# Kernel optimization log

Measured on AMD Instinct MI355X. Metric: run time of the kernel, lower is better.

Reference implementation:

```python
import jax, jax.numpy as jnp
import numpy as np

VOCAB, HID, EMB = 32000, 512, 100
DROPOUT = 0.3
BN_EPS = 1e-5


def setup_inputs() -> dict:
    key = jax.random.key(0)
    ks = jax.random.split(key, 12)
    B, T = 64, 512
    s = 1.0 / np.sqrt(HID)
    inp = {
        "x": jax.random.randint(ks[0], (B, T), 0, VOCAB),
        "emb_table": jax.random.normal(ks[1], (VOCAB, HID), jnp.float32) * 0.1,
        # PyTorch LSTMCell layout: weight_ih [4H, H], weight_hh [4H, H], gate order i,f,g,o
        "w_ih": jax.random.uniform(ks[2], (4 * HID, HID), jnp.float32, -s, s),
        "w_hh": jax.random.uniform(ks[3], (4 * HID, HID), jnp.float32, -s, s),
        "b_ih": jax.random.uniform(ks[4], (4 * HID,), jnp.float32, -s, s),
        "b_hh": jax.random.uniform(ks[5], (4 * HID,), jnp.float32, -s, s),
        "gamma": jnp.ones((HID,), jnp.float32),
        "beta": jnp.zeros((HID,), jnp.float32),
        "dec_w": jax.random.uniform(ks[6], (EMB, HID), jnp.float32, -s, s),
        "dec_b": jax.random.uniform(ks[7], (EMB,), jnp.float32, -s, s),
        # LockedDropout: one bernoulli(keep) mask shared across all timesteps
        "mask": jax.random.bernoulli(ks[8], 1.0 - DROPOUT, (B, HID)).astype(jnp.float32),
    }
    return inp


def reference(x, emb_table, w_ih, w_hh, b_ih, b_hh, gamma, beta, dec_w, dec_b, mask):
    embed = emb_table[x]                    # [B, T, H]
    xs = jnp.swapaxes(embed, 0, 1)          # [T, B, H]
    B = x.shape[0]
    keep = 1.0 - DROPOUT

    def step(carry, x_t):
        h, c = carry
        gates = x_t @ w_ih.T + b_ih + h @ w_hh.T + b_hh     # [B, 4H]
        i, f, g, o = jnp.split(gates, 4, axis=-1)
        i = jax.nn.sigmoid(i)
        f = jax.nn.sigmoid(f)
        g = jnp.tanh(g)
        o = jax.nn.sigmoid(o)
        c = f * c + i * g
        h = o * jnp.tanh(c)
        # BatchNorm1d in training mode: per-step batch stats (biased variance)
        mu = jnp.mean(h, axis=0)
        var = jnp.mean((h - mu) ** 2, axis=0)
        hn = (h - mu) * jax.lax.rsqrt(var + BN_EPS) * gamma + beta
        hd = hn * mask / keep                # LockedDropout, fixed mask
        out = hd @ dec_w.T + dec_b           # [B, EMB]
        return (h, c), out

    h0 = jnp.zeros((B, HID), embed.dtype)
    c0 = jnp.zeros((B, HID), embed.dtype)
    _, outs = jax.lax.scan(step, (h0, c0), xs)   # [T, B, EMB]
    # MaxPool1d with kernel == T over time axis -> max over T
    return jnp.max(outs, axis=0)                  # [B, EMB]
```

## Files before the change

### kernel.cpp

```cpp
#include <hip/hip_runtime.h>
#include <hip/hip_bf16.h>

#define TSEQ  512
#define BATCH 64
#define HIDN  512
#define EMBD  100
#define NWG   64

typedef __attribute__((ext_vector_type(8))) short short8;
typedef __attribute__((ext_vector_type(4))) float f32x4;
typedef unsigned int u32;

#define A_OFF   0ull
#define HD_OFF  33554432ull
#define HB_OFF  67108864ull
#define FLG_OFF 67239936ull
#define KEY_OFF 67244032ull
#define DW_OFF  67269632ull
#define ZERO_SPAN 160768ull

static __device__ __forceinline__ unsigned short f2bfbits(float f) {
    u32 u = __float_as_uint(f);
    u32 r = (u + 0x7fffu + ((u >> 16) & 1u)) >> 16;
    return (unsigned short)r;
}

static __device__ __forceinline__ float sigf(float x) {
    return __builtin_amdgcn_rcpf(1.0f + __expf(-x));
}
static __device__ __forceinline__ float tanhfast(float x) {
    float t = __expf(-2.0f * fabsf(x));
    float r = (1.0f - t) * __builtin_amdgcn_rcpf(1.0f + t);
    return copysignf(r, x);
}

__global__ void k_dw(const float* __restrict__ dw, unsigned short* __restrict__ dwb) {
    int i = blockIdx.x * 256 + threadIdx.x;
    float v = (i < EMBD * HIDN) ? dw[i] : 0.0f;
    dwb[i] = f2bfbits(v);
}

__global__ void k_embed(const int* __restrict__ x, const float* __restrict__ emb,
                        unsigned short* __restrict__ A) {
    int g = blockIdx.x * 256 + threadIdx.x;
    int k8 = g & 63;
    int bt = g >> 6;
    int b  = bt & 63;
    int t  = bt >> 6;
    int row = x[b * TSEQ + t];
    const float4* src = reinterpret_cast<const float4*>(emb + (size_t)row * HIDN + k8 * 8);
    float4 v0 = src[0], v1 = src[1];
    short8 s;
    s[0] = (short)f2bfbits(v0.x); s[1] = (short)f2bfbits(v0.y);
    s[2] = (short)f2bfbits(v0.z); s[3] = (short)f2bfbits(v0.w);
    s[4] = (short)f2bfbits(v1.x); s[5] = (short)f2bfbits(v1.y);
    s[6] = (short)f2bfbits(v1.z); s[7] = (short)f2bfbits(v1.w);
    *reinterpret_cast<short8*>(A + (size_t)g * 8) = s;
}

__launch_bounds__(512)
__global__ void k_lstm(const float* __restrict__ wih, const float* __restrict__ whh,
                       const float* __restrict__ bih, const float* __restrict__ bhh,
                       const float* __restrict__ gamma, const float* __restrict__ beta,
                       const float* __restrict__ mask,
                       const unsigned short* __restrict__ A,
                       unsigned short* __restrict__ hbuf,
                       unsigned short* __restrict__ hd,
                       u32* __restrict__ flg) {
    const int tid  = threadIdx.x;
    const int wg   = blockIdx.x;
    const int lane = tid & 63;
    const int w    = tid >> 6;
    const int mb   = w & 3;
    const int kh   = w >> 2;

    __shared__ float gbuf[2][64][33];
    __shared__ __align__(16) unsigned short hstage[64][8];
    __shared__ __align__(16) unsigned short hdstage[2][64][8];

    const int l15 = lane & 15;
    const int lk8 = (lane >> 4) * 8;

    const float* wsrc = kh ? whh : wih;
    short8 bfr[16][2];
    #pragma unroll
    for (int kk = 0; kk < 16; ++kk) {
        #pragma unroll
        for (int nb = 0; nb < 2; ++nb) {
            int nl   = nb * 16 + l15;
            int gate = nl >> 3, jl = nl & 7;
            int ng   = gate * HIDN + wg * 8 + jl;
            int kl   = kk * 32 + lk8;
            const float* p = wsrc + (size_t)ng * HIDN + kl;
            short8 bb;
            #pragma unroll
            for (int e = 0; e < 8; ++e) bb[e] = (short)f2bfbits(p[e]);
            bfr[kk][nb] = bb;
        }
    }

    const int jj = wg * 8 + w;
    const float bias_i = bih[jj]          + bhh[jj];
    const float bias_f = bih[512 + jj]    + bhh[512 + jj];
    const float bias_g = bih[1024 + jj]   + bhh[1024 + jj];
    const float bias_o = bih[1536 + jj]   + bhh[1536 + jj];
    const float gam = gamma[jj], bet = beta[jj];
    const float mk  = mask[(size_t)lane * HIDN + jj] * (1.0f / 0.7f);
    float c = 0.0f;

    const int arow = mb * 16 + l15;
    const u32* fp = flg + lane * 16;

    {
        float* g1 = &gbuf[1][0][0];
        for (int i = tid; i < 64 * 33; i += 512) g1[i] = 0.0f;
    }
    __syncthreads();
    if (kh == 0) {
        const unsigned short* abase = A + (size_t)arow * HIDN;
        f32x4 acc0 = {0.f,0.f,0.f,0.f}, acc1 = {0.f,0.f,0.f,0.f};
        #pragma unroll
        for (int kk = 0; kk < 16; ++kk) {
            short8 a = *reinterpret_cast<const short8*>(abase + kk * 32 + lk8);
            acc0 = __builtin_amdgcn_mfma_f32_16x16x32_bf16(a, bfr[kk][0], acc0, 0, 0, 0);
            acc1 = __builtin_amdgcn_mfma_f32_16x16x32_bf16(a, bfr[kk][1], acc1, 0, 0, 0);
        }
        #pragma unroll
        for (int r = 0; r < 4; ++r) {
            int row = mb * 16 + (lane >> 4) * 4 + r;
            gbuf[0][row][l15]      = acc0[r];
            gbuf[0][row][16 + l15] = acc1[r];
        }
    }
    __syncthreads();

    for (int s = 0; s < TSEQ; ++s) {
        float gi = gbuf[0][lane][w]      + gbuf[1][lane][w]      + bias_i;
        float gf = gbuf[0][lane][8 + w]  + gbuf[1][lane][8 + w]  + bias_f;
        float gg = gbuf[0][lane][16 + w] + gbuf[1][lane][16 + w] + bias_g;
        float go = gbuf[0][lane][24 + w] + gbuf[1][lane][24 + w] + bias_o;
        float iv = sigf(gi), fv = sigf(gf), gv = tanhfast(gg), ov = sigf(go);
        c = fv * c + iv * gv;
        float h = ov * tanhfast(c);
        hstage[lane][w] = f2bfbits(h);
        __syncthreads();

        const int sb = (s + 1) & 1;

        if (s != TSEQ - 1 && w == 0) {
            short8 hv = *reinterpret_cast<const short8*>(&hstage[lane][0]);
            unsigned short* dst = hbuf + (size_t)sb * 32768 + (size_t)wg * 512 + lane * 8;
            asm volatile("global_store_dwordx4 %0, %1, off sc1" :: "v"(dst), "v"(hv) : "memory");
        }

        {
            float s1 = h, s2 = h * h;
            #pragma unroll
            for (int m = 1; m < 64; m <<= 1) {
                s1 += __shfl_xor(s1, m, 64);
                s2 += __shfl_xor(s2, m, 64);
            }
            float mu  = s1 * (1.0f / 64.0f);
            float var = s2 * (1.0f / 64.0f) - mu * mu;
            float hn  = (h - mu) * rsqrtf(var + 1e-5f) * gam + bet;
            hdstage[s & 1][lane][w] = f2bfbits(hn * mk);
        }

        if (s != TSEQ - 1 && w == 0) {
            asm volatile("s_waitcnt vmcnt(0)" ::: "memory");
            if (lane == 0) {
                u32 fv = (u32)(s + 1);
                const u32* myf = flg + wg * 16;
                asm volatile("global_store_dword %0, %1, off sc1" :: "v"(myf), "v"(fv) : "memory");
            }
        }

        if (s != TSEQ - 1) {
            if (kh == 0) {
                const unsigned short* abase = A + ((size_t)(s + 1) * 64 + arow) * HIDN;
                f32x4 acc0 = {0.f,0.f,0.f,0.f}, acc1 = {0.f,0.f,0.f,0.f};
                #pragma unroll
                for (int kk = 0; kk < 16; ++kk) {
                    short8 a = *reinterpret_cast<const short8*>(abase + kk * 32 + lk8);
                    acc0 = __builtin_amdgcn_mfma_f32_16x16x32_bf16(a, bfr[kk][0], acc0, 0, 0, 0);
                    acc1 = __builtin_amdgcn_mfma_f32_16x16x32_bf16(a, bfr[kk][1], acc1, 0, 0, 0);
                }
                #pragma unroll
                for (int r = 0; r < 4; ++r) {
                    int row = mb * 16 + (lane >> 4) * 4 + r;
                    gbuf[0][row][l15]      = acc0[r];
                    gbuf[0][row][16 + l15] = acc1[r];
                }
            } else {
                const u32 tgt = (u32)(s + 1);
                u32 v;
                do {
                    asm volatile("global_load_dword %0, %1, off sc1"
                                 : "=v"(v) : "v"(fp) : "memory");
                    asm volatile("s_waitcnt vmcnt(0)" ::: "memory");
                } while (!__all((int)(v >= tgt)));
                __builtin_amdgcn_sched_barrier(0);
                short8 hf[16];
                #pragma unroll
                for (int kk = 0; kk < 16; ++kk) {
                    const unsigned short* p = hbuf + (size_t)sb * 32768
                        + (size_t)(kk * 4 + (lane >> 4)) * 512 + arow * 8;
                    asm volatile("global_load_dwordx4 %0, %1, off sc1"
                                 : "=v"(hf[kk]) : "v"(p) : "memory");
                }
                asm volatile("s_waitcnt vmcnt(0)" ::: "memory");
                __builtin_amdgcn_sched_barrier(0);
                f32x4 acc0 = {0.f,0.f,0.f,0.f}, acc1 = {0.f,0.f,0.f,0.f};
                #pragma unroll
                for (int kk = 0; kk < 16; ++kk) {
                    acc0 = __builtin_amdgcn_mfma_f32_16x16x32_bf16(hf[kk], bfr[kk][0], acc0, 0, 0, 0);
                    acc1 = __builtin_amdgcn_mfma_f32_16x16x32_bf16(hf[kk], bfr[kk][1], acc1, 0, 0, 0);
                }
                #pragma unroll
                for (int r = 0; r < 4; ++r) {
                    int row = mb * 16 + (lane >> 4) * 4 + r;
                    gbuf[1][row][l15]      = acc0[r];
                    gbuf[1][row][16 + l15] = acc1[r];
                }
            }
        }
        __syncthreads();

        if (w == 1) {
            short8 dv = *reinterpret_cast<const short8*>(&hdstage[s & 1][lane][0]);
            *reinterpret_cast<short8*>(hd + ((size_t)s * 64 + lane) * HIDN + wg * 8) = dv;
        }
    }
}

__launch_bounds__(256)
__global__ void k_decode(const unsigned short* __restrict__ hd,
                         const unsigned short* __restrict__ dwb,
                         u32* __restrict__ key) {
    const int t    = blockIdx.x;
    const int tid  = threadIdx.x;
    const int lane = tid & 63;
    const int w    = tid >> 6;
    const int l15  = lane & 15;
    const int lk8  = (lane >> 4) * 8;
    const int brow = w * 16 + l15;

    const unsigned short* abase = hd + ((size_t)t * 64 + brow) * HIDN;
    f32x4 acc[7];
    #pragma unroll
    for (int nb = 0; nb < 7; ++nb) acc[nb] = (f32x4){0.f, 0.f, 0.f, 0.f};

    #pragma unroll
    for (int kk = 0; kk < 16; ++kk) {
        short8 a = *reinterpret_cast<const short8*>(abase + kk * 32 + lk8);
        #pragma unroll
        for (int nb = 0; nb < 7; ++nb) {
            short8 b = *reinterpret_cast<const short8*>(
                dwb + (size_t)(nb * 16 + l15) * HIDN + kk * 32 + lk8);
            acc[nb] = __builtin_amdgcn_mfma_f32_16x16x32_bf16(a, b, acc[nb], 0, 0, 0);
        }
    }
    #pragma unroll
    for (int nb = 0; nb < 7; ++nb) {
        int n = nb * 16 + l15;
        if (n < EMBD) {
            #pragma unroll
            for (int r = 0; r < 4; ++r) {
                int b = w * 16 + (lane >> 4) * 4 + r;
                u32 u  = __float_as_uint(acc[nb][r]);
                u32 kv = (u & 0x80000000u) ? ~u : (u | 0x80000000u);
                atomicMax(&key[b * EMBD + n], kv);
            }
        }
    }
}

__global__ void k_final(const u32* __restrict__ key, const float* __restrict__ db,
                        float* __restrict__ out) {
    int i = blockIdx.x * 256 + threadIdx.x;
    if (i < BATCH * EMBD) {
        u32 k = key[i];
        u32 u = (k & 0x80000000u) ? (k & 0x7fffffffu) : ~k;
        out[i] = __uint_as_float(u) + db[i % EMBD];
    }
}

extern "C" void kernel_launch(void* const* d_in, const int* in_sizes, int n_in,
                              void* d_out, int out_size, void* d_ws, size_t ws_size,
                              hipStream_t stream) {
    const int*   x   = (const int*)d_in[0];
    const float* emb = (const float*)d_in[1];
    const float* wih = (const float*)d_in[2];
    const float* whh = (const float*)d_in[3];
    const float* bih = (const float*)d_in[4];
    const float* bhh = (const float*)d_in[5];
    const float* gam = (const float*)d_in[6];
    const float* bet = (const float*)d_in[7];
    const float* dw  = (const float*)d_in[8];
    const float* db  = (const float*)d_in[9];
    const float* msk = (const float*)d_in[10];

    char* ws = (char*)d_ws;
    unsigned short* A   = (unsigned short*)(ws + A_OFF);
    unsigned short* hd  = (unsigned short*)(ws + HD_OFF);
    unsigned short* hb  = (unsigned short*)(ws + HB_OFF);
    u32*            flg = (u32*)(ws + FLG_OFF);
    u32*            key = (u32*)(ws + KEY_OFF);
    unsigned short* dwb = (unsigned short*)(ws + DW_OFF);

    hipMemsetAsync(ws + HB_OFF, 0, ZERO_SPAN, stream);
    k_dw    <<<224,  256, 0, stream>>>(dw, dwb);
    k_embed <<<8192, 256, 0, stream>>>(x, emb, A);
    k_lstm  <<<NWG,  512, 0, stream>>>(wih, whh, bih, bhh, gam, bet, msk, A, hb, hd, flg);
    k_decode<<<TSEQ, 256, 0, stream>>>(hd, dwb, key);
    k_final <<<25,   256, 0, stream>>>(key, db, (float*)d_out);
}
```

Before: 2.118 ms.

## Embed step tags in h exchange and split K across all waves

Each hidden-state word is now stored interleaved with the step number, so consumers can check tags on the data itself. That replaces a separate flag poll followed by a dependent load, and the per-workgroup flag remains only as a fallback after several retries. The work is also re-partitioned so all 8 waves each handle a quarter of K for both the input and recurrent GEMMs, instead of half the waves doing input and half doing recurrent. The next step's input loads and the h loads are issued early, before the batch-norm reduction. The exchange buffer doubles in size and the gate sum now reads four partial buffers, and the tag check relies on 16-byte stores being observed atomically.

```diff
diff --git a/kernel.cpp b/kernel.cpp
--- a/kernel.cpp
+++ b/kernel.cpp
@@ -10,14 +10,15 @@
 typedef __attribute__((ext_vector_type(8))) short short8;
 typedef __attribute__((ext_vector_type(4))) float f32x4;
 typedef unsigned int u32;
+typedef __attribute__((ext_vector_type(4))) u32 u32x4;
 
 #define A_OFF   0ull
 #define HD_OFF  33554432ull
 #define HB_OFF  67108864ull
-#define FLG_OFF 67239936ull
-#define KEY_OFF 67244032ull
-#define DW_OFF  67269632ull
-#define ZERO_SPAN 160768ull
+#define FLG_OFF 67371008ull
+#define KEY_OFF 67375104ull
+#define DW_OFF  67400704ull
+#define ZERO_SPAN 291840ull
 
 static __device__ __forceinline__ unsigned short f2bfbits(float f) {
     u32 u = __float_as_uint(f);
@@ -58,44 +59,45 @@
     *reinterpret_cast<short8*>(A + (size_t)g * 8) = s;
 }
 
-__launch_bounds__(512)
+__launch_bounds__(512, 1)
 __global__ void k_lstm(const float* __restrict__ wih, const float* __restrict__ whh,
                        const float* __restrict__ bih, const float* __restrict__ bhh,
                        const float* __restrict__ gamma, const float* __restrict__ beta,
                        const float* __restrict__ mask,
                        const unsigned short* __restrict__ A,
-                       unsigned short* __restrict__ hbuf,
+                       u32* __restrict__ hx,
                        unsigned short* __restrict__ hd,
                        u32* __restrict__ flg) {
     const int tid  = threadIdx.x;
     const int wg   = blockIdx.x;
     const int lane = tid & 63;
     const int w    = tid >> 6;
-    const int mb   = w & 3;
-    const int kh   = w >> 2;
-
-    __shared__ float gbuf[2][64][33];
+    const int mh   = w & 1;
+    const int kq   = w >> 1;
+
+    __shared__ float gbuf[4][64][33];
     __shared__ __align__(16) unsigned short hstage[64][8];
     __shared__ __align__(16) unsigned short hdstage[2][64][8];
 
     const int l15 = lane & 15;
     const int lk8 = (lane >> 4) * 8;
 
-    const float* wsrc = kh ? whh : wih;
-    short8 bfr[16][2];
-    #pragma unroll
-    for (int kk = 0; kk < 16; ++kk) {
+    short8 bfrA[4][2], bfrH[4][2];
+    #pragma unroll
+    for (int kk = 0; kk < 4; ++kk) {
         #pragma unroll
         for (int nb = 0; nb < 2; ++nb) {
             int nl   = nb * 16 + l15;
             int gate = nl >> 3, jl = nl & 7;
             int ng   = gate * HIDN + wg * 8 + jl;
-            int kl   = kk * 32 + lk8;
-            const float* p = wsrc + (size_t)ng * HIDN + kl;
-            short8 bb;
-            #pragma unroll
-            for (int e = 0; e < 8; ++e) bb[e] = (short)f2bfbits(p[e]);
-            bfr[kk][nb] = bb;
+            int kl   = kq * 128 + kk * 32 + lk8;
+            const float* pa = wih + (size_t)ng * HIDN + kl;
+            const float* ph = whh + (size_t)ng * HIDN + kl;
+            short8 ba, bh;
+            #pragma unroll
+            for (int e = 0; e < 8; ++e) { ba[e] = (short)f2bfbits(pa[e]); bh[e] = (short)f2bfbits(ph[e]); }
+            bfrA[kk][nb] = ba;
+            bfrH[kk][nb] = bh;
         }
     }
 
@@ -108,49 +110,80 @@
     const float mk  = mask[(size_t)lane * HIDN + jj] * (1.0f / 0.7f);
     float c = 0.0f;
 
-    const int arow = mb * 16 + l15;
-    const u32* fp = flg + lane * 16;
-
-    {
-        float* g1 = &gbuf[1][0][0];
-        for (int i = tid; i < 64 * 33; i += 512) g1[i] = 0.0f;
-    }
-    __syncthreads();
-    if (kh == 0) {
-        const unsigned short* abase = A + (size_t)arow * HIDN;
-        f32x4 acc0 = {0.f,0.f,0.f,0.f}, acc1 = {0.f,0.f,0.f,0.f};
+    const int arow0 = mh * 32 + l15;
+    const u32* fpoll = flg + lane * 16;
+
+    #pragma unroll
+    for (int f = 0; f < 2; ++f) {
+        const unsigned short* abase = A + (size_t)(arow0 + f * 16) * HIDN + kq * 128;
+        f32x4 a0 = {0.f,0.f,0.f,0.f}, a1 = {0.f,0.f,0.f,0.f};
         #pragma unroll
-        for (int kk = 0; kk < 16; ++kk) {
+        for (int kk = 0; kk < 4; ++kk) {
             short8 a = *reinterpret_cast<const short8*>(abase + kk * 32 + lk8);
-            acc0 = __builtin_amdgcn_mfma_f32_16x16x32_bf16(a, bfr[kk][0], acc0, 0, 0, 0);
-            acc1 = __builtin_amdgcn_mfma_f32_16x16x32_bf16(a, bfr[kk][1], acc1, 0, 0, 0);
+            a0 = __builtin_amdgcn_mfma_f32_16x16x32_bf16(a, bfrA[kk][0], a0, 0, 0, 0);
+            a1 = __builtin_amdgcn_mfma_f32_16x16x32_bf16(a, bfrA[kk][1], a1, 0, 0, 0);
         }
         #pragma unroll
         for (int r = 0; r < 4; ++r) {
-            int row = mb * 16 + (lane >> 4) * 4 + r;
-            gbuf[0][row][l15]      = acc0[r];
-            gbuf[0][row][16 + l15] = acc1[r];
+            int row = mh * 32 + f * 16 + (lane >> 4) * 4 + r;
+            gbuf[kq][row][l15]      = a0[r];
+            gbuf[kq][row][16 + l15] = a1[r];
         }
     }
     __syncthreads();
 
     for (int s = 0; s < TSEQ; ++s) {
-        float gi = gbuf[0][lane][w]      + gbuf[1][lane][w]      + bias_i;
-        float gf = gbuf[0][lane][8 + w]  + gbuf[1][lane][8 + w]  + bias_f;
-        float gg = gbuf[0][lane][16 + w] + gbuf[1][lane][16 + w] + bias_g;
-        float go = gbuf[0][lane][24 + w] + gbuf[1][lane][24 + w] + bias_o;
+        float gi = gbuf[0][lane][w]      + gbuf[1][lane][w]
+                 + gbuf[2][lane][w]      + gbuf[3][lane][w]      + bias_i;
+        float gf = gbuf[0][lane][8 + w]  + gbuf[1][lane][8 + w]
+                 + gbuf[2][lane][8 + w]  + gbuf[3][lane][8 + w]  + bias_f;
+        float gg = gbuf[0][lane][16 + w] + gbuf[1][lane][16 + w]
+                 + gbuf[2][lane][16 + w] + gbuf[3][lane][16 + w] + bias_g;
+        float go = gbuf[0][lane][24 + w] + gbuf[1][lane][24 + w]
+                 + gbuf[2][lane][24 + w] + gbuf[3][lane][24 + w] + bias_o;
         float iv = sigf(gi), fv = sigf(gf), gv = tanhfast(gg), ov = sigf(go);
         c = fv * c + iv * gv;
         float h = ov * tanhfast(c);
         hstage[lane][w] = f2bfbits(h);
         __syncthreads();
 
-        const int sb = (s + 1) & 1;
-
-        if (s != TSEQ - 1 && w == 0) {
-            short8 hv = *reinterpret_cast<const short8*>(&hstage[lane][0]);
-            unsigned short* dst = hbuf + (size_t)sb * 32768 + (size_t)wg * 512 + lane * 8;
-            asm volatile("global_store_dwordx4 %0, %1, off sc1" :: "v"(dst), "v"(hv) : "memory");
+        const int last = (s == TSEQ - 1);
+        const int sb   = (s + 1) & 1;
+        const u32 tgt  = (u32)(s + 1);
+
+        short8 af[4][2];
+        u32x4  g0[4][2], g1[4][2];
+
+        if (!last) {
+            if (w == 0) {
+                const u32* hrow = reinterpret_cast<const u32*>(&hstage[lane][0]);
+                u32 a0 = hrow[0], a1 = hrow[1], a2 = hrow[2], a3 = hrow[3];
+                u32x4 q0 = {a0, tgt, a1, tgt};
+                u32x4 q1 = {a2, tgt, a3, tgt};
+                u32* dst = hx + (((size_t)sb * NWG + wg) * 64 + lane) * 8;
+                asm volatile("global_store_dwordx4 %0, %1, off sc1" :: "v"(dst), "v"(q0) : "memory");
+                asm volatile("global_store_dwordx4 %0, %1, off sc1" :: "v"(dst + 4), "v"(q1) : "memory");
+            }
+            #pragma unroll
+            for (int f = 0; f < 2; ++f) {
+                const unsigned short* abase =
+                    A + ((size_t)(s + 1) * 64 + arow0 + f * 16) * HIDN + kq * 128;
+                #pragma unroll
+                for (int kk = 0; kk < 4; ++kk) {
+                    const unsigned short* p = abase + kk * 32 + lk8;
+                    asm volatile("global_load_dwordx4 %0, %1, off" : "=v"(af[kk][f]) : "v"(p) : "memory");
+                }
+            }
+            #pragma unroll
+            for (int f = 0; f < 2; ++f) {
+                #pragma unroll
+                for (int kk = 0; kk < 4; ++kk) {
+                    int wgp = kq * 16 + kk * 4 + (lane >> 4);
+                    const u32* p = hx + (((size_t)sb * NWG + wgp) * 64 + arow0 + f * 16) * 8;
+                    asm volatile("global_load_dwordx4 %0, %1, off sc1" : "=v"(g0[kk][f]) : "v"(p) : "memory");
+                    asm volatile("global_load_dwordx4 %0, %1, off sc1" : "=v"(g1[kk][f]) : "v"(p + 4) : "memory");
+                }
+            }
         }
 
         {
@@ -166,61 +199,101 @@
             hdstage[s & 1][lane][w] = f2bfbits(hn * mk);
         }
 
-        if (s != TSEQ - 1 && w == 0) {
+        if (!last) {
             asm volatile("s_waitcnt vmcnt(0)" ::: "memory");
-            if (lane == 0) {
-                u32 fv = (u32)(s + 1);
+            __builtin_amdgcn_sched_barrier(0);
+            if (w == 0 && lane == 0) {
                 const u32* myf = flg + wg * 16;
-                asm volatile("global_store_dword %0, %1, off sc1" :: "v"(myf), "v"(fv) : "memory");
-            }
-        }
-
-        if (s != TSEQ - 1) {
-            if (kh == 0) {
-                const unsigned short* abase = A + ((size_t)(s + 1) * 64 + arow) * HIDN;
-                f32x4 acc0 = {0.f,0.f,0.f,0.f}, acc1 = {0.f,0.f,0.f,0.f};
-                #pragma unroll
-                for (int kk = 0; kk < 16; ++kk) {
-                    short8 a = *reinterpret_cast<const short8*>(abase + kk * 32 + lk8);
-                    acc0 = __builtin_amdgcn_mfma_f32_16x16x32_bf16(a, bfr[kk][0], acc0, 0, 0, 0);
-                    acc1 = __builtin_amdgcn_mfma_f32_16x16x32_bf16(a, bfr[kk][1], acc1, 0, 0, 0);
-                }
-                #pragma unroll
-                for (int r = 0; r < 4; ++r) {
-                    int row = mb * 16 + (lane >> 4) * 4 + r;
-                    gbuf[0][row][l15]      = acc0[r];
-                    gbuf[0][row][16 + l15] = acc1[r];
-                }
-            } else {
-                const u32 tgt = (u32)(s + 1);
+                asm volatile("global_store_dword %0, %1, off sc1" :: "v"(myf), "v"(tgt) : "memory");
+            }
+
+            int ok;
+            {
+                int o = 1;
+                #pragma unroll
+                for (int f = 0; f < 2; ++f)
+                    #pragma unroll
+                    for (int kk = 0; kk < 4; ++kk)
+                        o &= (g0[kk][f].y == tgt) & (g0[kk][f].w == tgt)
+                           & (g1[kk][f].y == tgt) & (g1[kk][f].w == tgt);
+                ok = __all(o);
+            }
+            #pragma unroll 1
+            for (int att = 0; att < 6 && !ok; ++att) {
+                #pragma unroll
+                for (int f = 0; f < 2; ++f) {
+                    #pragma unroll
+                    for (int kk = 0; kk < 4; ++kk) {
+                        int wgp = kq * 16 + kk * 4 + (lane >> 4);
+                        const u32* p = hx + (((size_t)sb * NWG + wgp) * 64 + arow0 + f * 16) * 8;
+                        if ((g0[kk][f].y != tgt) | (g0[kk][f].w != tgt))
+                            asm volatile("global_load_dwordx4 %0, %1, off sc1" : "=v"(g0[kk][f]) : "v"(p) : "memory");
+                        if ((g1[kk][f].y != tgt) | (g1[kk][f].w != tgt))
+                            asm volatile("global_load_dwordx4 %0, %1, off sc1" : "=v"(g1[kk][f]) : "v"(p + 4) : "memory");
+                    }
+                }
+                asm volatile("s_waitcnt vmcnt(0)" ::: "memory");
+                __builtin_amdgcn_sched_barrier(0);
+                int o = 1;
+                #pragma unroll
+                for (int f = 0; f < 2; ++f)
+                    #pragma unroll
+                    for (int kk = 0; kk < 4; ++kk)
+                        o &= (g0[kk][f].y == tgt) & (g0[kk][f].w == tgt)
+                           & (g1[kk][f].y == tgt) & (g1[kk][f].w == tgt);
+                ok = __all(o);
+            }
+            if (!ok) {
                 u32 v;
                 do {
-                    asm volatile("global_load_dword %0, %1, off sc1"
-                                 : "=v"(v) : "v"(fp) : "memory");
+                    asm volatile("global_load_dword %0, %1, off sc1" : "=v"(v) : "v"(fpoll) : "memory");
                     asm volatile("s_waitcnt vmcnt(0)" ::: "memory");
                 } while (!__all((int)(v >= tgt)));
                 __builtin_amdgcn_sched_barrier(0);
-                short8 hf[16];
-                #pragma unroll
-                for (int kk = 0; kk < 16; ++kk) {
-                    const unsigned short* p = hbuf + (size_t)sb * 32768
-                        + (size_t)(kk * 4 + (lane >> 4)) * 512 + arow * 8;
-                    asm volatile("global_load_dwordx4 %0, %1, off sc1"
-                                 : "=v"(hf[kk]) : "v"(p) : "memory");
+                #pragma unroll
+                for (int f = 0; f < 2; ++f) {
+                    #pragma unroll
+                    for (int kk = 0; kk < 4; ++kk) {
+                        int wgp = kq * 16 + kk * 4 + (lane >> 4);
+                        const u32* p = hx + (((size_t)sb * NWG + wgp) * 64 + arow0 + f * 16) * 8;
+                        asm volatile("global_load_dwordx4 %0, %1, off sc1" : "=v"(g0[kk][f]) : "v"(p) : "memory");
+                        asm volatile("global_load_dwordx4 %0, %1, off sc1" : "=v"(g1[kk][f]) : "v"(p + 4) : "memory");
+                    }
                 }
                 asm volatile("s_waitcnt vmcnt(0)" ::: "memory");
                 __builtin_amdgcn_sched_barrier(0);
-                f32x4 acc0 = {0.f,0.f,0.f,0.f}, acc1 = {0.f,0.f,0.f,0.f};
-                #pragma unroll
-                for (int kk = 0; kk < 16; ++kk) {
-                    acc0 = __builtin_amdgcn_mfma_f32_16x16x32_bf16(hf[kk], bfr[kk][0], acc0, 0, 0, 0);
-                    acc1 = __builtin_amdgcn_mfma_f32_16x16x32_bf16(hf[kk], bfr[kk][1], acc1, 0, 0, 0);
-                }
+            }
+
+            f32x4 acc[2][2];
+            #pragma unroll
+            for (int f = 0; f < 2; ++f)
+                #pragma unroll
+                for (int nb = 0; nb < 2; ++nb) acc[f][nb] = (f32x4){0.f,0.f,0.f,0.f};
+            #pragma unroll
+            for (int f = 0; f < 2; ++f) {
+                #pragma unroll
+                for (int kk = 0; kk < 4; ++kk) {
+                    acc[f][0] = __builtin_amdgcn_mfma_f32_16x16x32_bf16(af[kk][f], bfrA[kk][0], acc[f][0], 0, 0, 0);
+                    acc[f][1] = __builtin_amdgcn_mfma_f32_16x16x32_bf16(af[kk][f], bfrA[kk][1], acc[f][1], 0, 0, 0);
+                }
+            }
+            #pragma unroll
+            for (int f = 0; f < 2; ++f) {
+                #pragma unroll
+                for (int kk = 0; kk < 4; ++kk) {
+                    u32x4 q = {g0[kk][f].x, g0[kk][f].z, g1[kk][f].x, g1[kk][f].z};
+                    short8 a = *reinterpret_cast<short8*>(&q);
+                    acc[f][0] = __builtin_amdgcn_mfma_f32_16x16x32_bf16(a, bfrH[kk][0], acc[f][0], 0, 0, 0);
+                    acc[f][1] = __builtin_amdgcn_mfma_f32_16x16x32_bf16(a, bfrH[kk][1], acc[f][1], 0, 0, 0);
+                }
+            }
+            #pragma unroll
+            for (int f = 0; f < 2; ++f) {
                 #pragma unroll
                 for (int r = 0; r < 4; ++r) {
-                    int row = mb * 16 + (lane >> 4) * 4 + r;
-                    gbuf[1][row][l15]      = acc0[r];
-                    gbuf[1][row][16 + l15] = acc1[r];
+                    int row = mh * 32 + f * 16 + (lane >> 4) * 4 + r;
+                    gbuf[kq][row][l15]      = acc[f][0][r];
+                    gbuf[kq][row][16 + l15] = acc[f][1][r];
                 }
             }
         }
@@ -303,7 +376,7 @@
     char* ws = (char*)d_ws;
     unsigned short* A   = (unsigned short*)(ws + A_OFF);
     unsigned short* hd  = (unsigned short*)(ws + HD_OFF);
-    unsigned short* hb  = (unsigned short*)(ws + HB_OFF);
+    u32*            hx  = (u32*)(ws + HB_OFF);
     u32*            flg = (u32*)(ws + FLG_OFF);
     u32*            key = (u32*)(ws + KEY_OFF);
     unsigned short* dwb = (unsigned short*)(ws + DW_OFF);
@@ -311,7 +384,7 @@
     hipMemsetAsync(ws + HB_OFF, 0, ZERO_SPAN, stream);
     k_dw    <<<224,  256, 0, stream>>>(dw, dwb);
     k_embed <<<8192, 256, 0, stream>>>(x, emb, A);
-    k_lstm  <<<NWG,  512, 0, stream>>>(wih, whh, bih, bhh, gam, bet, msk, A, hb, hd, flg);
+    k_lstm  <<<NWG,  512, 0, stream>>>(wih, whh, bih, bhh, gam, bet, msk, A, hx, hd, flg);
     k_decode<<<TSEQ, 256, 0, stream>>>(hd, dwb, key);
     k_final <<<25,   256, 0, stream>>>(key, db, (float*)d_out);
 }
```

After: 2.585 ms. 1.22x slower.

## Split LSTM workgroups by batch and hidden slices; move BatchNorm into decode kernel

Applied to the files above, without the earlier changes.

The recurrent kernel now gives each workgroup 16 batch rows and 32 hidden units across all four gates, instead of 8 hidden units for all 64 batch rows. Each workgroup then only waits on the 16 peers that share its batch slice rather than all 64. The per-step BatchNorm and dropout, which needed a cross-batch reduction, move out of the serial loop. A new k_bnd kernel computes per-timestep batch statistics from bf16 hidden states in shared memory before the decoder GEMM. The trade-off is that BN statistics now come from bf16-rounded h, and the decode kernel does extra shared-memory and normalisation work.

```diff
diff --git a/kernel.cpp b/kernel.cpp
--- a/kernel.cpp
+++ b/kernel.cpp
@@ -24,7 +24,9 @@
     u32 r = (u + 0x7fffu + ((u >> 16) & 1u)) >> 16;
     return (unsigned short)r;
 }
-
+static __device__ __forceinline__ float bf2f(unsigned short b) {
+    return __uint_as_float(((u32)b) << 16);
+}
 static __device__ __forceinline__ float sigf(float x) {
     return __builtin_amdgcn_rcpf(1.0f + __expf(-x));
 }
@@ -61,22 +63,21 @@
 __launch_bounds__(512)
 __global__ void k_lstm(const float* __restrict__ wih, const float* __restrict__ whh,
                        const float* __restrict__ bih, const float* __restrict__ bhh,
-                       const float* __restrict__ gamma, const float* __restrict__ beta,
-                       const float* __restrict__ mask,
                        const unsigned short* __restrict__ A,
                        unsigned short* __restrict__ hbuf,
                        unsigned short* __restrict__ hd,
                        u32* __restrict__ flg) {
     const int tid  = threadIdx.x;
     const int wg   = blockIdx.x;
+    const int g    = wg & 3;
+    const int m    = wg >> 2;
     const int lane = tid & 63;
     const int w    = tid >> 6;
-    const int mb   = w & 3;
+    const int nbw  = w & 3;
     const int kh   = w >> 2;
 
-    __shared__ float gbuf[2][64][33];
-    __shared__ __align__(16) unsigned short hstage[64][8];
-    __shared__ __align__(16) unsigned short hdstage[2][64][8];
+    __shared__ float gbuf[2][16][132];
+    __shared__ __align__(16) unsigned short hstage[2][16][32];
 
     const int l15 = lane & 15;
     const int lk8 = (lane >> 4) * 8;
@@ -87,11 +88,8 @@
     for (int kk = 0; kk < 16; ++kk) {
         #pragma unroll
         for (int nb = 0; nb < 2; ++nb) {
-            int nl   = nb * 16 + l15;
-            int gate = nl >> 3, jl = nl & 7;
-            int ng   = gate * HIDN + wg * 8 + jl;
-            int kl   = kk * 32 + lk8;
-            const float* p = wsrc + (size_t)ng * HIDN + kl;
+            int jrow = nbw * HIDN + m * 32 + nb * 16 + l15;
+            const float* p = wsrc + (size_t)jrow * HIDN + kk * 32 + lk8;
             short8 bb;
             #pragma unroll
             for (int e = 0; e < 8; ++e) bb[e] = (short)f2bfbits(p[e]);
@@ -99,160 +97,178 @@
         }
     }
 
-    const int jj = wg * 8 + w;
-    const float bias_i = bih[jj]          + bhh[jj];
-    const float bias_f = bih[512 + jj]    + bhh[512 + jj];
-    const float bias_g = bih[1024 + jj]   + bhh[1024 + jj];
-    const float bias_o = bih[1536 + jj]   + bhh[1536 + jj];
-    const float gam = gamma[jj], bet = beta[jj];
-    const float mk  = mask[(size_t)lane * HIDN + jj] * (1.0f / 0.7f);
+    const int prow = tid >> 5;
+    const int pcol = tid & 31;
+    const int jj   = m * 32 + pcol;
+    const float bias_i = bih[jj]           + bhh[jj];
+    const float bias_f = bih[512 + jj]     + bhh[512 + jj];
+    const float bias_g = bih[1024 + jj]    + bhh[1024 + jj];
+    const float bias_o = bih[1536 + jj]    + bhh[1536 + jj];
     float c = 0.0f;
 
-    const int arow = mb * 16 + l15;
-    const u32* fp = flg + lane * 16;
+    const int arow = g * 16 + l15;
+    const u32* fpoll = flg + ((size_t)g * 16 + (lane & 15)) * 16;
 
     {
         float* g1 = &gbuf[1][0][0];
-        for (int i = tid; i < 64 * 33; i += 512) g1[i] = 0.0f;
+        for (int i = tid; i < 16 * 132; i += 512) g1[i] = 0.0f;
     }
     __syncthreads();
     if (kh == 0) {
         const unsigned short* abase = A + (size_t)arow * HIDN;
-        f32x4 acc0 = {0.f,0.f,0.f,0.f}, acc1 = {0.f,0.f,0.f,0.f};
+        f32x4 a0 = {0.f,0.f,0.f,0.f}, a1 = {0.f,0.f,0.f,0.f};
         #pragma unroll
         for (int kk = 0; kk < 16; ++kk) {
             short8 a = *reinterpret_cast<const short8*>(abase + kk * 32 + lk8);
-            acc0 = __builtin_amdgcn_mfma_f32_16x16x32_bf16(a, bfr[kk][0], acc0, 0, 0, 0);
-            acc1 = __builtin_amdgcn_mfma_f32_16x16x32_bf16(a, bfr[kk][1], acc1, 0, 0, 0);
+            a0 = __builtin_amdgcn_mfma_f32_16x16x32_bf16(a, bfr[kk][0], a0, 0, 0, 0);
+            a1 = __builtin_amdgcn_mfma_f32_16x16x32_bf16(a, bfr[kk][1], a1, 0, 0, 0);
         }
         #pragma unroll
         for (int r = 0; r < 4; ++r) {
-            int row = mb * 16 + (lane >> 4) * 4 + r;
-            gbuf[0][row][l15]      = acc0[r];
-            gbuf[0][row][16 + l15] = acc1[r];
+            int crow = (lane >> 4) * 4 + r;
+            gbuf[0][crow][nbw * 32 + l15]      = a0[r];
+            gbuf[0][crow][nbw * 32 + 16 + l15] = a1[r];
         }
     }
     __syncthreads();
 
     for (int s = 0; s < TSEQ; ++s) {
-        float gi = gbuf[0][lane][w]      + gbuf[1][lane][w]      + bias_i;
-        float gf = gbuf[0][lane][8 + w]  + gbuf[1][lane][8 + w]  + bias_f;
-        float gg = gbuf[0][lane][16 + w] + gbuf[1][lane][16 + w] + bias_g;
-        float go = gbuf[0][lane][24 + w] + gbuf[1][lane][24 + w] + bias_o;
+        float gi = gbuf[0][prow][pcol]      + gbuf[1][prow][pcol]      + bias_i;
+        float gf = gbuf[0][prow][32 + pcol] + gbuf[1][prow][32 + pcol] + bias_f;
+        float gg = gbuf[0][prow][64 + pcol] + gbuf[1][prow][64 + pcol] + bias_g;
+        float go = gbuf[0][prow][96 + pcol] + gbuf[1][prow][96 + pcol] + bias_o;
         float iv = sigf(gi), fv = sigf(gf), gv = tanhfast(gg), ov = sigf(go);
         c = fv * c + iv * gv;
         float h = ov * tanhfast(c);
-        hstage[lane][w] = f2bfbits(h);
+        hstage[s & 1][prow][pcol] = f2bfbits(h);
         __syncthreads();
 
-        const int sb = (s + 1) & 1;
-
-        if (s != TSEQ - 1 && w == 0) {
-            short8 hv = *reinterpret_cast<const short8*>(&hstage[lane][0]);
-            unsigned short* dst = hbuf + (size_t)sb * 32768 + (size_t)wg * 512 + lane * 8;
+        const int last = (s == TSEQ - 1);
+        const int sb   = (s + 1) & 1;
+        const u32 tgt  = (u32)(s + 1);
+
+        if (!last && w == 0) {
+            int r0 = lane >> 2, pc = (lane & 3) * 8;
+            short8 hv = *reinterpret_cast<const short8*>(&hstage[s & 1][r0][pc]);
+            unsigned short* dst = hbuf + ((size_t)(sb * 4 + g) * 16 + r0) * HIDN + m * 32 + pc;
             asm volatile("global_store_dwordx4 %0, %1, off sc1" :: "v"(dst), "v"(hv) : "memory");
-        }
-
-        {
-            float s1 = h, s2 = h * h;
-            #pragma unroll
-            for (int m = 1; m < 64; m <<= 1) {
-                s1 += __shfl_xor(s1, m, 64);
-                s2 += __shfl_xor(s2, m, 64);
-            }
-            float mu  = s1 * (1.0f / 64.0f);
-            float var = s2 * (1.0f / 64.0f) - mu * mu;
-            float hn  = (h - mu) * rsqrtf(var + 1e-5f) * gam + bet;
-            hdstage[s & 1][lane][w] = f2bfbits(hn * mk);
-        }
-
-        if (s != TSEQ - 1 && w == 0) {
             asm volatile("s_waitcnt vmcnt(0)" ::: "memory");
             if (lane == 0) {
-                u32 fv = (u32)(s + 1);
-                const u32* myf = flg + wg * 16;
-                asm volatile("global_store_dword %0, %1, off sc1" :: "v"(myf), "v"(fv) : "memory");
+                const u32* myf = flg + ((size_t)g * 16 + m) * 16;
+                asm volatile("global_store_dword %0, %1, off sc1" :: "v"(myf), "v"(tgt) : "memory");
             }
         }
 
-        if (s != TSEQ - 1) {
+        if (w == 1) {
+            int r0 = lane >> 2, pc = (lane & 3) * 8;
+            short8 dv = *reinterpret_cast<const short8*>(&hstage[s & 1][r0][pc]);
+            *reinterpret_cast<short8*>(
+                hd + ((size_t)s * 64 + g * 16 + r0) * HIDN + m * 32 + pc) = dv;
+        }
+
+        if (!last) {
             if (kh == 0) {
                 const unsigned short* abase = A + ((size_t)(s + 1) * 64 + arow) * HIDN;
-                f32x4 acc0 = {0.f,0.f,0.f,0.f}, acc1 = {0.f,0.f,0.f,0.f};
+                f32x4 a0 = {0.f,0.f,0.f,0.f}, a1 = {0.f,0.f,0.f,0.f};
                 #pragma unroll
                 for (int kk = 0; kk < 16; ++kk) {
                     short8 a = *reinterpret_cast<const short8*>(abase + kk * 32 + lk8);
-                    acc0 = __builtin_amdgcn_mfma_f32_16x16x32_bf16(a, bfr[kk][0], acc0, 0, 0, 0);
-                    acc1 = __builtin_amdgcn_mfma_f32_16x16x32_bf16(a, bfr[kk][1], acc1, 0, 0, 0);
+                    a0 = __builtin_amdgcn_mfma_f32_16x16x32_bf16(a, bfr[kk][0], a0, 0, 0, 0);
+                    a1 = __builtin_amdgcn_mfma_f32_16x16x32_bf16(a, bfr[kk][1], a1, 0, 0, 0);
                 }
                 #pragma unroll
                 for (int r = 0; r < 4; ++r) {
-                    int row = mb * 16 + (lane >> 4) * 4 + r;
-                    gbuf[0][row][l15]      = acc0[r];
-                    gbuf[0][row][16 + l15] = acc1[r];
+                    int crow = (lane >> 4) * 4 + r;
+                    gbuf[0][crow][nbw * 32 + l15]      = a0[r];
+                    gbuf[0][crow][nbw * 32 + 16 + l15] = a1[r];
                 }
             } else {
-                const u32 tgt = (u32)(s + 1);
                 u32 v;
                 do {
                     asm volatile("global_load_dword %0, %1, off sc1"
-                                 : "=v"(v) : "v"(fp) : "memory");
+                                 : "=v"(v) : "v"(fpoll) : "memory");
                     asm volatile("s_waitcnt vmcnt(0)" ::: "memory");
                 } while (!__all((int)(v >= tgt)));
                 __builtin_amdgcn_sched_barrier(0);
+                const unsigned short* hbase = hbuf + ((size_t)(sb * 4 + g) * 16 + l15) * HIDN;
                 short8 hf[16];
                 #pragma unroll
                 for (int kk = 0; kk < 16; ++kk) {
-                    const unsigned short* p = hbuf + (size_t)sb * 32768
-                        + (size_t)(kk * 4 + (lane >> 4)) * 512 + arow * 8;
+                    const unsigned short* p = hbase + kk * 32 + lk8;
                     asm volatile("global_load_dwordx4 %0, %1, off sc1"
                                  : "=v"(hf[kk]) : "v"(p) : "memory");
                 }
                 asm volatile("s_waitcnt vmcnt(0)" ::: "memory");
                 __builtin_amdgcn_sched_barrier(0);
-                f32x4 acc0 = {0.f,0.f,0.f,0.f}, acc1 = {0.f,0.f,0.f,0.f};
+                f32x4 a0 = {0.f,0.f,0.f,0.f}, a1 = {0.f,0.f,0.f,0.f};
                 #pragma unroll
                 for (int kk = 0; kk < 16; ++kk) {
-                    acc0 = __builtin_amdgcn_mfma_f32_16x16x32_bf16(hf[kk], bfr[kk][0], acc0, 0, 0, 0);
-                    acc1 = __builtin_amdgcn_mfma_f32_16x16x32_bf16(hf[kk], bfr[kk][1], acc1, 0, 0, 0);
+                    a0 = __builtin_amdgcn_mfma_f32_16x16x32_bf16(hf[kk], bfr[kk][0], a0, 0, 0, 0);
+                    a1 = __builtin_amdgcn_mfma_f32_16x16x32_bf16(hf[kk], bfr[kk][1], a1, 0, 0, 0);
                 }
                 #pragma unroll
                 for (int r = 0; r < 4; ++r) {
-                    int row = mb * 16 + (lane >> 4) * 4 + r;
-                    gbuf[1][row][l15]      = acc0[r];
-                    gbuf[1][row][16 + l15] = acc1[r];
+                    int crow = (lane >> 4) * 4 + r;
+                    gbuf[1][crow][nbw * 32 + l15]      = a0[r];
+                    gbuf[1][crow][nbw * 32 + 16 + l15] = a1[r];
                 }
             }
         }
         __syncthreads();
-
-        if (w == 1) {
-            short8 dv = *reinterpret_cast<const short8*>(&hdstage[s & 1][lane][0]);
-            *reinterpret_cast<short8*>(hd + ((size_t)s * 64 + lane) * HIDN + wg * 8) = dv;
-        }
     }
 }
 
 __launch_bounds__(256)
-__global__ void k_decode(const unsigned short* __restrict__ hd,
-                         const unsigned short* __restrict__ dwb,
-                         u32* __restrict__ key) {
-    const int t    = blockIdx.x;
-    const int tid  = threadIdx.x;
+__global__ void k_bnd(const unsigned short* __restrict__ hd,
+                      const unsigned short* __restrict__ dwb,
+                      const float* __restrict__ gamma, const float* __restrict__ beta,
+                      const float* __restrict__ mask,
+                      u32* __restrict__ key) {
+    const int t   = blockIdx.x;
+    const int tid = threadIdx.x;
+    __shared__ __align__(16) unsigned short hs[64][520];
+
+    for (int ch = tid; ch < 4096; ch += 256) {
+        int row = ch >> 6, c8 = (ch & 63) * 8;
+        short8 v = *reinterpret_cast<const short8*>(hd + ((size_t)t * 64 + row) * HIDN + c8);
+        *reinterpret_cast<short8*>(&hs[row][c8]) = v;
+    }
+    __syncthreads();
+
+    {
+        int c0 = tid * 2;
+        float s10 = 0.f, s20 = 0.f, s11 = 0.f, s21 = 0.f;
+        for (int r = 0; r < 64; ++r) {
+            float x0 = bf2f(hs[r][c0]), x1 = bf2f(hs[r][c0 + 1]);
+            s10 += x0; s20 += x0 * x0;
+            s11 += x1; s21 += x1 * x1;
+        }
+        float mu0 = s10 * (1.0f / 64.0f), var0 = s20 * (1.0f / 64.0f) - mu0 * mu0;
+        float mu1 = s11 * (1.0f / 64.0f), var1 = s21 * (1.0f / 64.0f) - mu1 * mu1;
+        float sc0 = gamma[c0]     * rsqrtf(var0 + 1e-5f);
+        float sc1 = gamma[c0 + 1] * rsqrtf(var1 + 1e-5f);
+        float sh0 = beta[c0]     - mu0 * sc0;
+        float sh1 = beta[c0 + 1] - mu1 * sc1;
+        for (int r = 0; r < 64; ++r) {
+            float2 mk = *reinterpret_cast<const float2*>(&mask[(size_t)r * HIDN + c0]);
+            float y0 = (bf2f(hs[r][c0])     * sc0 + sh0) * mk.x * (1.0f / 0.7f);
+            float y1 = (bf2f(hs[r][c0 + 1]) * sc1 + sh1) * mk.y * (1.0f / 0.7f);
+            hs[r][c0]     = f2bfbits(y0);
+            hs[r][c0 + 1] = f2bfbits(y1);
+        }
+    }
+    __syncthreads();
+
     const int lane = tid & 63;
     const int w    = tid >> 6;
     const int l15  = lane & 15;
     const int lk8  = (lane >> 4) * 8;
-    const int brow = w * 16 + l15;
-
-    const unsigned short* abase = hd + ((size_t)t * 64 + brow) * HIDN;
     f32x4 acc[7];
     #pragma unroll
     for (int nb = 0; nb < 7; ++nb) acc[nb] = (f32x4){0.f, 0.f, 0.f, 0.f};
-
     #pragma unroll
     for (int kk = 0; kk < 16; ++kk) {
-        short8 a = *reinterpret_cast<const short8*>(abase + kk * 32 + lk8);
+        short8 a = *reinterpret_cast<const short8*>(&hs[w * 16 + l15][kk * 32 + lk8]);
         #pragma unroll
         for (int nb = 0; nb < 7; ++nb) {
             short8 b = *reinterpret_cast<const short8*>(
@@ -311,7 +327,7 @@
     hipMemsetAsync(ws + HB_OFF, 0, ZERO_SPAN, stream);
     k_dw    <<<224,  256, 0, stream>>>(dw, dwb);
     k_embed <<<8192, 256, 0, stream>>>(x, emb, A);
-    k_lstm  <<<NWG,  512, 0, stream>>>(wih, whh, bih, bhh, gam, bet, msk, A, hb, hd, flg);
-    k_decode<<<TSEQ, 256, 0, stream>>>(hd, dwb, key);
+    k_lstm  <<<NWG,  512, 0, stream>>>(wih, whh, bih, bhh, A, hb, hd, flg);
+    k_bnd   <<<TSEQ, 256, 0, stream>>>(hd, dwb, gam, bet, msk, key);
     k_final <<<25,   256, 0, stream>>>(key, db, (float*)d_out);
 }
```

Measured after the change: 2.588 ms. 22.2% more time.

## Embed step tags in exchanged hidden state to replace flag polling

Applied to the files above, without the earlier changes.

The hidden-state exchange between workgroups now interleaves each pair of bf16 values with the step counter in the same 16-byte store. Readers load the data eagerly and check the embedded tags, so they can skip the separate flag poll and its extra round trip, falling back to flag polling only after a few failed retries. All eight waves cooperatively load the full h into a new LDS buffer, and the recurrent MFMA reads from LDS. The cost is doubled exchange traffic, a larger LDS footprint, and an extra barrier per step; correctness relies on 16-byte stores being seen atomically.

```diff
diff --git a/kernel.cpp b/kernel.cpp
--- a/kernel.cpp
+++ b/kernel.cpp
@@ -10,21 +10,22 @@
 typedef __attribute__((ext_vector_type(8))) short short8;
 typedef __attribute__((ext_vector_type(4))) float f32x4;
 typedef unsigned int u32;
+typedef __attribute__((ext_vector_type(4))) u32 u32x4;
+typedef __attribute__((ext_vector_type(2))) u32 u32x2;
 
 #define A_OFF   0ull
 #define HD_OFF  33554432ull
 #define HB_OFF  67108864ull
-#define FLG_OFF 67239936ull
-#define KEY_OFF 67244032ull
-#define DW_OFF  67269632ull
-#define ZERO_SPAN 160768ull
+#define FLG_OFF 67371008ull
+#define KEY_OFF 67375104ull
+#define DW_OFF  67400704ull
+#define ZERO_SPAN 291840ull
 
 static __device__ __forceinline__ unsigned short f2bfbits(float f) {
     u32 u = __float_as_uint(f);
     u32 r = (u + 0x7fffu + ((u >> 16) & 1u)) >> 16;
     return (unsigned short)r;
 }
-
 static __device__ __forceinline__ float sigf(float x) {
     return __builtin_amdgcn_rcpf(1.0f + __expf(-x));
 }
@@ -64,7 +65,7 @@
                        const float* __restrict__ gamma, const float* __restrict__ beta,
                        const float* __restrict__ mask,
                        const unsigned short* __restrict__ A,
-                       unsigned short* __restrict__ hbuf,
+                       u32* __restrict__ hx,
                        unsigned short* __restrict__ hd,
                        u32* __restrict__ flg) {
     const int tid  = threadIdx.x;
@@ -77,6 +78,7 @@
     __shared__ float gbuf[2][64][33];
     __shared__ __align__(16) unsigned short hstage[64][8];
     __shared__ __align__(16) unsigned short hdstage[2][64][8];
+    __shared__ __align__(16) unsigned short h_lds[64][520];
 
     const int l15 = lane & 15;
     const int lk8 = (lane >> 4) * 8;
@@ -109,7 +111,7 @@
     float c = 0.0f;
 
     const int arow = mb * 16 + l15;
-    const u32* fp = flg + lane * 16;
+    const u32* fpoll = flg + lane * 16;
 
     {
         float* g1 = &gbuf[1][0][0];
@@ -118,18 +120,18 @@
     __syncthreads();
     if (kh == 0) {
         const unsigned short* abase = A + (size_t)arow * HIDN;
-        f32x4 acc0 = {0.f,0.f,0.f,0.f}, acc1 = {0.f,0.f,0.f,0.f};
+        f32x4 a0 = {0.f,0.f,0.f,0.f}, a1 = {0.f,0.f,0.f,0.f};
         #pragma unroll
         for (int kk = 0; kk < 16; ++kk) {
             short8 a = *reinterpret_cast<const short8*>(abase + kk * 32 + lk8);
-            acc0 = __builtin_amdgcn_mfma_f32_16x16x32_bf16(a, bfr[kk][0], acc0, 0, 0, 0);
-            acc1 = __builtin_amdgcn_mfma_f32_16x16x32_bf16(a, bfr[kk][1], acc1, 0, 0, 0);
+            a0 = __builtin_amdgcn_mfma_f32_16x16x32_bf16(a, bfr[kk][0], a0, 0, 0, 0);
+            a1 = __builtin_amdgcn_mfma_f32_16x16x32_bf16(a, bfr[kk][1], a1, 0, 0, 0);
         }
         #pragma unroll
         for (int r = 0; r < 4; ++r) {
             int row = mb * 16 + (lane >> 4) * 4 + r;
-            gbuf[0][row][l15]      = acc0[r];
-            gbuf[0][row][16 + l15] = acc1[r];
+            gbuf[0][row][l15]      = a0[r];
+            gbuf[0][row][16 + l15] = a1[r];
         }
     }
     __syncthreads();
@@ -145,12 +147,28 @@
         hstage[lane][w] = f2bfbits(h);
         __syncthreads();
 
-        const int sb = (s + 1) & 1;
-
-        if (s != TSEQ - 1 && w == 0) {
-            short8 hv = *reinterpret_cast<const short8*>(&hstage[lane][0]);
-            unsigned short* dst = hbuf + (size_t)sb * 32768 + (size_t)wg * 512 + lane * 8;
-            asm volatile("global_store_dwordx4 %0, %1, off sc1" :: "v"(dst), "v"(hv) : "memory");
+        const int last = (s == TSEQ - 1);
+        const int sb   = (s + 1) & 1;
+        const u32 tgt  = (u32)(s + 1);
+
+        u32x4 gq[16];
+        const u32* gp = hx + ((size_t)sb * 64 + lane) * 512 + w * 64;
+
+        if (!last) {
+            if (w == 0) {
+                const u32* hrow = reinterpret_cast<const u32*>(&hstage[lane][0]);
+                u32 d0 = hrow[0], d1 = hrow[1], d2 = hrow[2], d3 = hrow[3];
+                u32x4 q0 = {d0, tgt, d1, tgt};
+                u32x4 q1 = {d2, tgt, d3, tgt};
+                u32* dst = hx + ((size_t)sb * 64 + lane) * 512 + wg * 8;
+                asm volatile("global_store_dwordx4 %0, %1, off sc1" :: "v"(dst), "v"(q0) : "memory");
+                asm volatile("global_store_dwordx4 %0, %1, off sc1" :: "v"(dst + 4), "v"(q1) : "memory");
+            }
+            #pragma unroll
+            for (int i = 0; i < 16; ++i) {
+                asm volatile("global_load_dwordx4 %0, %1, off sc1"
+                             : "=v"(gq[i]) : "v"(gp + i * 4) : "memory");
+            }
         }
 
         {
@@ -166,61 +184,87 @@
             hdstage[s & 1][lane][w] = f2bfbits(hn * mk);
         }
 
-        if (s != TSEQ - 1 && w == 0) {
+        if (!last) {
             asm volatile("s_waitcnt vmcnt(0)" ::: "memory");
-            if (lane == 0) {
-                u32 fv = (u32)(s + 1);
+            __builtin_amdgcn_sched_barrier(0);
+            if (w == 0 && lane == 0) {
                 const u32* myf = flg + wg * 16;
-                asm volatile("global_store_dword %0, %1, off sc1" :: "v"(myf), "v"(fv) : "memory");
-            }
-        }
-
-        if (s != TSEQ - 1) {
-            if (kh == 0) {
-                const unsigned short* abase = A + ((size_t)(s + 1) * 64 + arow) * HIDN;
-                f32x4 acc0 = {0.f,0.f,0.f,0.f}, acc1 = {0.f,0.f,0.f,0.f};
-                #pragma unroll
-                for (int kk = 0; kk < 16; ++kk) {
-                    short8 a = *reinterpret_cast<const short8*>(abase + kk * 32 + lk8);
-                    acc0 = __builtin_amdgcn_mfma_f32_16x16x32_bf16(a, bfr[kk][0], acc0, 0, 0, 0);
-                    acc1 = __builtin_amdgcn_mfma_f32_16x16x32_bf16(a, bfr[kk][1], acc1, 0, 0, 0);
-                }
-                #pragma unroll
-                for (int r = 0; r < 4; ++r) {
-                    int row = mb * 16 + (lane >> 4) * 4 + r;
-                    gbuf[0][row][l15]      = acc0[r];
-                    gbuf[0][row][16 + l15] = acc1[r];
-                }
-            } else {
-                const u32 tgt = (u32)(s + 1);
+                asm volatile("global_store_dword %0, %1, off sc1" :: "v"(myf), "v"(tgt) : "memory");
+            }
+            int ok;
+            {
+                int o = 1;
+                #pragma unroll
+                for (int i = 0; i < 16; ++i) o &= (gq[i].y == tgt) & (gq[i].w == tgt);
+                ok = __all(o);
+            }
+            #pragma unroll 1
+            for (int att = 0; att < 4 && !ok; ++att) {
+                #pragma unroll
+                for (int i = 0; i < 16; ++i) {
+                    if ((gq[i].y != tgt) | (gq[i].w != tgt))
+                        asm volatile("global_load_dwordx4 %0, %1, off sc1"
+                                     : "=v"(gq[i]) : "v"(gp + i * 4) : "memory");
+                }
+                asm volatile("s_waitcnt vmcnt(0)" ::: "memory");
+                __builtin_amdgcn_sched_barrier(0);
+                int o = 1;
+                #pragma unroll
+                for (int i = 0; i < 16; ++i) o &= (gq[i].y == tgt) & (gq[i].w == tgt);
+                ok = __all(o);
+            }
+            if (!ok) {
                 u32 v;
                 do {
                     asm volatile("global_load_dword %0, %1, off sc1"
-                                 : "=v"(v) : "v"(fp) : "memory");
+                                 : "=v"(v) : "v"(fpoll) : "memory");
                     asm volatile("s_waitcnt vmcnt(0)" ::: "memory");
                 } while (!__all((int)(v >= tgt)));
                 __builtin_amdgcn_sched_barrier(0);
-                short8 hf[16];
-                #pragma unroll
-                for (int kk = 0; kk < 16; ++kk) {
-                    const unsigned short* p = hbuf + (size_t)sb * 32768
-                        + (size_t)(kk * 4 + (lane >> 4)) * 512 + arow * 8;
+                #pragma unroll
+                for (int i = 0; i < 16; ++i)
                     asm volatile("global_load_dwordx4 %0, %1, off sc1"
-                                 : "=v"(hf[kk]) : "v"(p) : "memory");
-                }
+                                 : "=v"(gq[i]) : "v"(gp + i * 4) : "memory");
                 asm volatile("s_waitcnt vmcnt(0)" ::: "memory");
                 __builtin_amdgcn_sched_barrier(0);
-                f32x4 acc0 = {0.f,0.f,0.f,0.f}, acc1 = {0.f,0.f,0.f,0.f};
+            }
+            #pragma unroll
+            for (int i = 0; i < 16; ++i) {
+                u32x2 d = {gq[i].x, gq[i].z};
+                *reinterpret_cast<u32x2*>(&h_lds[lane][(w * 16 + i) * 4]) = d;
+            }
+        }
+        __syncthreads();
+
+        if (!last) {
+            if (kh == 0) {
+                const unsigned short* abase = A + ((size_t)(s + 1) * 64 + arow) * HIDN;
+                f32x4 a0 = {0.f,0.f,0.f,0.f}, a1 = {0.f,0.f,0.f,0.f};
                 #pragma unroll
                 for (int kk = 0; kk < 16; ++kk) {
-                    acc0 = __builtin_amdgcn_mfma_f32_16x16x32_bf16(hf[kk], bfr[kk][0], acc0, 0, 0, 0);
-                    acc1 = __builtin_amdgcn_mfma_f32_16x16x32_bf16(hf[kk], bfr[kk][1], acc1, 0, 0, 0);
+                    short8 a = *reinterpret_cast<const short8*>(abase + kk * 32 + lk8);
+                    a0 = __builtin_amdgcn_mfma_f32_16x16x32_bf16(a, bfr[kk][0], a0, 0, 0, 0);
+                    a1 = __builtin_amdgcn_mfma_f32_16x16x32_bf16(a, bfr[kk][1], a1, 0, 0, 0);
                 }
                 #pragma unroll
                 for (int r = 0; r < 4; ++r) {
                     int row = mb * 16 + (lane >> 4) * 4 + r;
-                    gbuf[1][row][l15]      = acc0[r];
-                    gbuf[1][row][16 + l15] = acc1[r];
+                    gbuf[0][row][l15]      = a0[r];
+                    gbuf[0][row][16 + l15] = a1[r];
+                }
+            } else {
+                f32x4 a0 = {0.f,0.f,0.f,0.f}, a1 = {0.f,0.f,0.f,0.f};
+                #pragma unroll
+                for (int kk = 0; kk < 16; ++kk) {
+                    short8 a = *reinterpret_cast<const short8*>(&h_lds[arow][kk * 32 + lk8]);
+                    a0 = __builtin_amdgcn_mfma_f32_16x16x32_bf16(a, bfr[kk][0], a0, 0, 0, 0);
+                    a1 = __builtin_amdgcn_mfma_f32_16x16x32_bf16(a, bfr[kk][1], a1, 0, 0, 0);
+                }
+                #pragma unroll
+                for (int r = 0; r < 4; ++r) {
+                    int row = mb * 16 + (lane >> 4) * 4 + r;
+                    gbuf[1][row][l15]      = a0[r];
+                    gbuf[1][row][16 + l15] = a1[r];
                 }
             }
         }
@@ -303,7 +347,7 @@
     char* ws = (char*)d_ws;
     unsigned short* A   = (unsigned short*)(ws + A_OFF);
     unsigned short* hd  = (unsigned short*)(ws + HD_OFF);
-    unsigned short* hb  = (unsigned short*)(ws + HB_OFF);
+    u32*            hx  = (u32*)(ws + HB_OFF);
     u32*            flg = (u32*)(ws + FLG_OFF);
     u32*            key = (u32*)(ws + KEY_OFF);
     unsigned short* dwb = (unsigned short*)(ws + DW_OFF);
@@ -311,7 +355,7 @@
     hipMemsetAsync(ws + HB_OFF, 0, ZERO_SPAN, stream);
     k_dw    <<<224,  256, 0, stream>>>(dw, dwb);
     k_embed <<<8192, 256, 0, stream>>>(x, emb, A);
-    k_lstm  <<<NWG,  512, 0, stream>>>(wih, whh, bih, bhh, gam, bet, msk, A, hb, hd, flg);
+    k_lstm  <<<NWG,  512, 0, stream>>>(wih, whh, bih, bhh, gam, bet, msk, A, hx, hd, flg);
     k_decode<<<TSEQ, 256, 0, stream>>>(hd, dwb, key);
     k_final <<<25,   256, 0, stream>>>(key, db, (float*)d_out);
 }
```

New measurement: 6.749 ms. +218.7%, slower.
